# Performance work log

Hardware: AMD Instinct MI355X
Metric: run time of the kernel (lower is better)

## Reference

```python
import jax, jax.numpy as jnp
import numpy as np

N_ATOMS, N_UND, N_DIR, N_ANG, N_STRUCT = 8192, 65536, 131072, 262144, 128
FEA, NRAD, NANGB, NCONV = 64, 9, 9, 4

FLOAT_NAMES = ["bond_bases_ag", "bond_bases_bg", "angle_bases", "atom_emb", "Wb", "Wa",
               "Wbw_ag", "Wbw_bg",
               "ac_cw1", "ac_cb1", "ac_cw2", "ac_cb2", "ac_gw1", "ac_gb1", "ac_gw2", "ac_gb2", "ac_out",
               "bc_cw1", "bc_cb1", "bc_cw2", "bc_cb2", "bc_gw1", "bc_gb1", "bc_gw2", "bc_gb2", "bc_out",
               "an_cw", "an_cb", "an_gw", "an_gb",
               "ro_w1", "ro_b1", "ro_w2", "ro_b2", "ro_w3", "ro_b3"]
INT_NAMES = ["atomic_numbers", "atom_graph", "directed2undirected",
             "bond_graph_atoms", "bond_graph_bonds", "atom_owners"]


def _silu(x):
    return x * jax.nn.sigmoid(x)


def _gmlp(x, cw1, cb1, cw2, cb2, gw1, gb1, gw2, gb2):
    # GatedMLP (norm=None): silu(MLP_core(x)) * sigmoid(MLP_gate(x)), each MLP = Lin-silu-Lin
    core = _silu(_silu(x @ cw1 + cb1) @ cw2 + cb2)
    gate = jax.nn.sigmoid(_silu(x @ gw1 + gb1) @ gw2 + gb2)
    return core * gate


def _forward(F, I):
    seg = jax.ops.segment_sum
    atom = F["atom_emb"][I["atomic_numbers"]]            # [N, 64]
    bond = F["bond_bases_ag"] @ F["Wb"]                  # [U, 64]
    angle = F["angle_bases"] @ F["Wa"]                   # [A, 64]
    bw_ag = F["bond_bases_ag"] @ F["Wbw_ag"]             # [U, 64]
    bw_bg = F["bond_bases_bg"] @ F["Wbw_bg"]             # [U, 64]
    ag0, ag1 = I["atom_graph"][:, 0], I["atom_graph"][:, 1]
    d2u = I["directed2undirected"]
    bgi, bgj = I["bond_graph_bonds"][:, 0], I["bond_graph_bonds"][:, 1]
    bga = I["bond_graph_atoms"]

    def atom_conv(i, atom, bond):
        msg = jnp.concatenate([atom[ag0], bond[d2u], atom[ag1]], axis=1)   # [E, 192]
        msg = _gmlp(msg, F["ac_cw1"][i], F["ac_cb1"][i], F["ac_cw2"][i], F["ac_cb2"][i],
                    F["ac_gw1"][i], F["ac_gb1"][i], F["ac_gw2"][i], F["ac_gb2"][i])
        msg = msg * bw_ag[d2u]
        # scatter-add to center atoms, linear mlp_out (no bias), resnet
        return atom + seg(msg, ag0, num_segments=N_ATOMS) @ F["ac_out"][i]

    for i in range(NCONV - 1):
        atom = atom_conv(i, atom, bond)
        # BondConv over bond graph (angles)
        tot = jnp.concatenate([bond[bgi], bond[bgj], angle, atom[bga]], axis=1)  # [A, 256]
        upd = _gmlp(tot, F["bc_cw1"][i], F["bc_cb1"][i], F["bc_cw2"][i], F["bc_cb2"][i],
                    F["bc_gw1"][i], F["bc_gb1"][i], F["bc_gw2"][i], F["bc_gb2"][i])
        upd = upd * bw_bg[bgi]
        bond = bond + seg(upd, bgi, num_segments=N_UND) @ F["bc_out"][i]
        # AngleUpdate (hidden_dim=0 -> single linear in each gated branch), resnet
        tot2 = jnp.concatenate([bond[bgi], bond[bgj], angle, atom[bga]], axis=1)
        angle = angle + _silu(tot2 @ F["an_cw"][i] + F["an_cb"][i]) * \
            jax.nn.sigmoid(tot2 @ F["an_gw"][i] + F["an_gb"][i])
    atom = atom_conv(NCONV - 1, atom, bond)

    # mlp_first readout: per-atom energy MLP then average pooling per structure
    e = _silu(atom @ F["ro_w1"] + F["ro_b1"])
    e = _silu(e @ F["ro_w2"] + F["ro_b2"])
    e = (e @ F["ro_w3"] + F["ro_b3"])[:, 0]              # [N]
    owners = I["atom_owners"]
    esum = seg(e, owners, num_segments=N_STRUCT)
    cnt = seg(jnp.ones_like(e), owners, num_segments=N_STRUCT)
    return esum / jnp.maximum(cnt, 1.0)                  # [N_STRUCT] energy/atom


def setup_inputs() -> dict:
    key = jax.random.key(0)
    ks = iter(jax.random.split(key, 64))

    def nrm(shape, fan_in):
        return jax.random.normal(next(ks), shape, dtype=jnp.float32) / np.float32(np.sqrt(fan_in))

    z = lambda *s: jnp.zeros(s, dtype=jnp.float32)
    inp = {}
    inp["atomic_numbers"] = jax.random.randint(next(ks), (N_ATOMS,), 0, 94, dtype=jnp.int32)
    inp["bond_bases_ag"] = jax.random.uniform(next(ks), (N_UND, NRAD), dtype=jnp.float32)
    inp["bond_bases_bg"] = jax.random.uniform(next(ks), (N_UND, NRAD), dtype=jnp.float32)
    inp["angle_bases"] = jax.random.uniform(next(ks), (N_ANG, NANGB), dtype=jnp.float32)
    inp["atom_graph"] = jax.random.randint(next(ks), (N_DIR, 2), 0, N_ATOMS, dtype=jnp.int32)
    inp["directed2undirected"] = jax.random.randint(next(ks), (N_DIR,), 0, N_UND, dtype=jnp.int32)
    inp["bond_graph_atoms"] = jax.random.randint(next(ks), (N_ANG,), 0, N_ATOMS, dtype=jnp.int32)
    inp["bond_graph_bonds"] = jax.random.randint(next(ks), (N_ANG, 2), 0, N_UND, dtype=jnp.int32)
    inp["atom_owners"] = jnp.sort(jax.random.randint(next(ks), (N_ATOMS,), 0, N_STRUCT, dtype=jnp.int32))
    inp["atom_emb"] = nrm((95, FEA), 1.0)
    inp["Wb"] = nrm((NRAD, FEA), NRAD)
    inp["Wa"] = nrm((NANGB, FEA), NANGB)
    inp["Wbw_ag"] = nrm((NRAD, FEA), NRAD)
    inp["Wbw_bg"] = nrm((NRAD, FEA), NRAD)
    d_a, d_b = 3 * FEA, 4 * FEA
    nb = NCONV - 1
    inp["ac_cw1"] = nrm((NCONV, d_a, FEA), d_a); inp["ac_cb1"] = z(NCONV, FEA)
    inp["ac_cw2"] = nrm((NCONV, FEA, FEA), FEA); inp["ac_cb2"] = z(NCONV, FEA)
    inp["ac_gw1"] = nrm((NCONV, d_a, FEA), d_a); inp["ac_gb1"] = z(NCONV, FEA)
    inp["ac_gw2"] = nrm((NCONV, FEA, FEA), FEA); inp["ac_gb2"] = z(NCONV, FEA)
    inp["ac_out"] = nrm((NCONV, FEA, FEA), FEA)
    inp["bc_cw1"] = nrm((nb, d_b, FEA), d_b); inp["bc_cb1"] = z(nb, FEA)
    inp["bc_cw2"] = nrm((nb, FEA, FEA), FEA); inp["bc_cb2"] = z(nb, FEA)
    inp["bc_gw1"] = nrm((nb, d_b, FEA), d_b); inp["bc_gb1"] = z(nb, FEA)
    inp["bc_gw2"] = nrm((nb, FEA, FEA), FEA); inp["bc_gb2"] = z(nb, FEA)
    inp["bc_out"] = nrm((nb, FEA, FEA), FEA)
    inp["an_cw"] = nrm((nb, d_b, FEA), d_b); inp["an_cb"] = z(nb, FEA)
    inp["an_gw"] = nrm((nb, d_b, FEA), d_b); inp["an_gb"] = z(nb, FEA)
    inp["ro_w1"] = nrm((FEA, FEA), FEA); inp["ro_b1"] = z(FEA)
    inp["ro_w2"] = nrm((FEA, FEA), FEA); inp["ro_b2"] = z(FEA)
    inp["ro_w3"] = nrm((FEA, 1), FEA); inp["ro_b3"] = z(1)
    return inp


def reference(atomic_numbers, bond_bases_ag, bond_bases_bg, angle_bases, atom_graph,
              directed2undirected, bond_graph_atoms, bond_graph_bonds, atom_owners,
              atom_emb, Wb, Wa, Wbw_ag, Wbw_bg,
              ac_cw1, ac_cb1, ac_cw2, ac_cb2, ac_gw1, ac_gb1, ac_gw2, ac_gb2, ac_out,
              bc_cw1, bc_cb1, bc_cw2, bc_cb2, bc_gw1, bc_gb1, bc_gw2, bc_gb2, bc_out,
              an_cw, an_cb, an_gw, an_gb,
              ro_w1, ro_b1, ro_w2, ro_b2, ro_w3, ro_b3):
    loc = locals()
    F = {k: loc[k] for k in FLOAT_NAMES}
    I = {k: loc[k] for k in INT_NAMES}
    return _forward(F, I)
```

## Files before the change

### kernel.cpp

```cpp
#include <hip/hip_runtime.h>
#include <hip/hip_bf16.h>

typedef float f32x4 __attribute__((ext_vector_type(4)));
typedef short s16x8 __attribute__((ext_vector_type(8)));
typedef unsigned int u32x4 __attribute__((ext_vector_type(4)));

#define DEV static __device__ __forceinline__

DEV unsigned short f2bf(float x){
    unsigned u = __builtin_bit_cast(unsigned, x);
    u += 0x7FFFu + ((u >> 16) & 1u);
    return (unsigned short)(u >> 16);
}
DEV float bf2f(unsigned short h){
    unsigned u = ((unsigned)h) << 16;
    return __builtin_bit_cast(float, u);
}
DEV float sigm_(float x){ return __builtin_amdgcn_rcpf(1.0f + __expf(-x)); }
DEV float silu_(float x){ return x * sigm_(x); }

__global__ __launch_bounds__(256) void k_transconv(const float* __restrict__ src,
                                                   unsigned short* __restrict__ dst,
                                                   int K, int total){
    int gid = blockIdx.x * 256 + threadIdx.x;
    if (gid >= total) return;
    int kn  = K * 64;
    int b   = gid / kn;
    int rem = gid - b * kn;
    int k   = rem >> 6, n = rem & 63;
    dst[b * kn + n * K + k] = f2bf(src[gid]);
}

__global__ __launch_bounds__(256) void k_embed(const float* __restrict__ emb,
                                               const int* __restrict__ z,
                                               unsigned short* __restrict__ out){
    int gid = blockIdx.x * 256 + threadIdx.x;
    int n = gid >> 6, f = gid & 63;
    out[gid] = f2bf(emb[z[n] * 64 + f]);
}

__global__ __launch_bounds__(256) void k_smallmm(const float* __restrict__ bases,
                                                 const float* __restrict__ W,
                                                 unsigned short* __restrict__ out){
    int gid = blockIdx.x * 256 + threadIdx.x;
    int r = gid >> 6, f = gid & 63;
    const float* b = bases + r * 9;
    float acc = 0.f;
    #pragma unroll
    for (int k = 0; k < 9; ++k) acc += b[k] * W[k * 64 + f];
    out[gid] = f2bf(acc);
}

__global__ void k_count(const int* __restrict__ dst, int stride, int n, int* __restrict__ cnt){
    int i = blockIdx.x * 256 + threadIdx.x;
    if (i < n) atomicAdd(&cnt[dst[(size_t)i * stride]], 1);
}

__global__ __launch_bounds__(256) void k_bsum(const int* __restrict__ cnt,
                                              int* __restrict__ bsum){
    int i = blockIdx.x * 256 + threadIdx.x;
    int v = cnt[i];
    #pragma unroll
    for (int off = 32; off > 0; off >>= 1) v += __shfl_down(v, off);
    __shared__ int ws[4];
    if ((threadIdx.x & 63) == 0) ws[threadIdx.x >> 6] = v;
    __syncthreads();
    if (threadIdx.x == 0) bsum[blockIdx.x] = ws[0] + ws[1] + ws[2] + ws[3];
}

__global__ __launch_bounds__(256) void k_bscan(const int* __restrict__ bsum,
                                               int* __restrict__ bbase, int nb,
                                               int* __restrict__ total_out){
    __shared__ int sh[256];
    int t = threadIdx.x;
    int v = (t < nb) ? bsum[t] : 0;
    sh[t] = v;
    __syncthreads();
    for (int d = 1; d < 256; d <<= 1){
        int u = (t >= d) ? sh[t - d] : 0;
        __syncthreads();
        sh[t] += u;
        __syncthreads();
    }
    if (t < nb) bbase[t] = sh[t] - v;
    if (t == nb - 1) *total_out = sh[t];
}

__global__ __launch_bounds__(256) void k_offs(const int* __restrict__ cnt,
                                              const int* __restrict__ bbase,
                                              int* __restrict__ offs){
    __shared__ int sh[256];
    int t = threadIdx.x;
    int i = blockIdx.x * 256 + t;
    int v = cnt[i];
    sh[t] = v;
    __syncthreads();
    for (int d = 1; d < 256; d <<= 1){
        int u = (t >= d) ? sh[t - d] : 0;
        __syncthreads();
        sh[t] += u;
        __syncthreads();
    }
    offs[i] = bbase[blockIdx.x] + sh[t] - v;
}

__global__ void k_fill(const int* __restrict__ dst, int stride, int n,
                       const int* __restrict__ offs, int* __restrict__ cur,
                       int* __restrict__ idx){
    int i = blockIdx.x * 256 + threadIdx.x;
    if (i < n){
        int d = dst[(size_t)i * stride];
        int p = offs[d] + atomicAdd(&cur[d], 1);
        idx[p] = i;
    }
}

__global__ __launch_bounds__(256) void k_reduce(const unsigned short* __restrict__ upd,
                                                const int* __restrict__ offs,
                                                const int* __restrict__ idx,
                                                unsigned short* __restrict__ act, int nRows){
    int gid = blockIdx.x * 256 + threadIdx.x;
    int row = gid >> 3;
    if (row >= nRows) return;
    int c8 = (gid & 7) * 8;
    int o = offs[row], e = offs[row + 1];
    float acc[8] = {};
    for (int j = o; j < e; ++j){
        s16x8 v = *(const s16x8*)&upd[(size_t)idx[j] * 64 + c8];
        #pragma unroll
        for (int q = 0; q < 8; ++q) acc[q] += bf2f((unsigned short)v[q]);
    }
    s16x8 a = *(s16x8*)&act[(size_t)row * 64 + c8];
    #pragma unroll
    for (int q = 0; q < 8; ++q) a[q] = (short)f2bf(bf2f((unsigned short)a[q]) + acc[q]);
    *(s16x8*)&act[(size_t)row * 64 + c8] = a;
}

#define MFMA16(a,b,c) __builtin_amdgcn_mfma_f32_16x16x32_bf16(a,b,c,0,0,0)

__global__ __launch_bounds__(256, 4) void k_atom_conv(
    const unsigned short* __restrict__ atomBf, const unsigned short* __restrict__ bondBf,
    const unsigned short* __restrict__ bwagBf,
    const int* __restrict__ agraph, const int* __restrict__ d2u,
    const unsigned short* __restrict__ w1cT, const unsigned short* __restrict__ w1gT,
    const unsigned short* __restrict__ w2cT, const unsigned short* __restrict__ w2gT,
    const unsigned short* __restrict__ woT,
    const float* __restrict__ cb1, const float* __restrict__ cb2,
    const float* __restrict__ gb1, const float* __restrict__ gb2,
    unsigned short* __restrict__ upd)
{
    __shared__ unsigned short lds[14208];
    __shared__ int ldsIdx[64];
    unsigned short* ldsA  = lds;
    unsigned short* ldsHC = lds;
    unsigned short* ldsHG = lds + 4736;
    unsigned short* ldsV  = lds + 9472;
    const int tid = threadIdx.x;
    const int r0  = blockIdx.x * 64;

    {
        const int srow = tid >> 2, q = tid & 3;
        int e = r0 + srow;
        if (q < 3){
            const unsigned short* src;
            if (q == 0)      src = atomBf + (size_t)agraph[2 * e] * 64;
            else if (q == 1){ int u = d2u[e]; ldsIdx[srow] = u; src = bondBf + (size_t)u * 64; }
            else             src = atomBf + (size_t)agraph[2 * e + 1] * 64;
            #pragma unroll
            for (int j = 0; j < 8; ++j)
                *(u32x4*)&ldsA[srow * 200 + q * 64 + j * 8] = *(const u32x4*)(src + j * 8);
        }
    }
    __syncthreads();

    const int lane = tid & 63;
    const int r16  = lane & 15;
    const int grp  = lane >> 4;
    const int col  = (tid >> 6) * 16 + r16;

    unsigned short bwv[16];
    #pragma unroll
    for (int mt = 0; mt < 4; ++mt)
        #pragma unroll
        for (int j = 0; j < 4; ++j)
            bwv[mt * 4 + j] = bwagBf[(size_t)ldsIdx[mt * 16 + grp * 4 + j] * 64 + col];

    f32x4 aC[4] = {}, aG[4] = {};
    #pragma unroll
    for (int kt = 0; kt < 6; ++kt){
        s16x8 bc = *(const s16x8*)&w1cT[col * 192 + kt * 32 + grp * 8];
        s16x8 bg = *(const s16x8*)&w1gT[col * 192 + kt * 32 + grp * 8];
        #pragma unroll
        for (int mt = 0; mt < 4; ++mt){
            s16x8 a = *(const s16x8*)&ldsA[(mt * 16 + r16) * 200 + kt * 32 + grp * 8];
            aC[mt] = MFMA16(a, bc, aC[mt]);
            aG[mt] = MFMA16(a, bg, aG[mt]);
        }
    }
    __syncthreads();

    const float bC1 = cb1[col], bG1 = gb1[col];
    #pragma unroll
    for (int mt = 0; mt < 4; ++mt){
        #pragma unroll
        for (int j = 0; j < 4; ++j){
            int row = mt * 16 + grp * 4 + j;
            ldsHC[row * 74 + col] = f2bf(silu_(aC[mt][j] + bC1));
            ldsHG[row * 74 + col] = f2bf(silu_(aG[mt][j] + bG1));
        }
    }
    __syncthreads();

    f32x4 oC[4] = {}, oG[4] = {};
    #pragma unroll
    for (int kt = 0; kt < 2; ++kt){
        s16x8 bc = *(const s16x8*)&w2cT[col * 64 + kt * 32 + grp * 8];
        s16x8 bg = *(const s16x8*)&w2gT[col * 64 + kt * 32 + grp * 8];
        #pragma unroll
        for (int mt = 0; mt < 4; ++mt){
            s16x8 hc = *(const s16x8*)&ldsHC[(mt * 16 + r16) * 74 + kt * 32 + grp * 8];
            s16x8 hg = *(const s16x8*)&ldsHG[(mt * 16 + r16) * 74 + kt * 32 + grp * 8];
            oC[mt] = MFMA16(hc, bc, oC[mt]);
            oG[mt] = MFMA16(hg, bg, oG[mt]);
        }
    }
    const float bC2 = cb2[col], bG2 = gb2[col];
    #pragma unroll
    for (int mt = 0; mt < 4; ++mt){
        #pragma unroll
        for (int j = 0; j < 4; ++j){
            int row = mt * 16 + grp * 4 + j;
            float v = silu_(oC[mt][j] + bC2) * sigm_(oG[mt][j] + bG2);
            v *= bf2f(bwv[mt * 4 + j]);
            ldsV[row * 74 + col] = f2bf(v);
        }
    }
    __syncthreads();

    f32x4 oD[4] = {};
    #pragma unroll
    for (int kt = 0; kt < 2; ++kt){
        s16x8 bo = *(const s16x8*)&woT[col * 64 + kt * 32 + grp * 8];
        #pragma unroll
        for (int mt = 0; mt < 4; ++mt){
            s16x8 a = *(const s16x8*)&ldsV[(mt * 16 + r16) * 74 + kt * 32 + grp * 8];
            oD[mt] = MFMA16(a, bo, oD[mt]);
        }
    }
    #pragma unroll
    for (int mt = 0; mt < 4; ++mt){
        #pragma unroll
        for (int j = 0; j < 4; ++j){
            int row = mt * 16 + grp * 4 + j;
            upd[(size_t)(r0 + row) * 64 + col] = f2bf(oD[mt][j]);
        }
    }
}

__global__ __launch_bounds__(256, 4) void k_bond_conv(
    const unsigned short* __restrict__ atomBf, const unsigned short* __restrict__ bondBf,
    const unsigned short* __restrict__ angleBf, const unsigned short* __restrict__ bwbgBf,
    const int* __restrict__ bga, const int* __restrict__ bgb,
    const unsigned short* __restrict__ w1cT, const unsigned short* __restrict__ w1gT,
    const unsigned short* __restrict__ w2cT, const unsigned short* __restrict__ w2gT,
    const unsigned short* __restrict__ woT,
    const float* __restrict__ cb1, const float* __restrict__ cb2,
    const float* __restrict__ gb1, const float* __restrict__ gb2,
    unsigned short* __restrict__ upd)
{
    __shared__ unsigned short lds[16896];
    __shared__ int ldsIdx[64];
    unsigned short* ldsA  = lds;
    unsigned short* ldsHC = lds;
    unsigned short* ldsHG = lds + 4736;
    unsigned short* ldsV  = lds + 9472;
    const int tid = threadIdx.x;
    const int r0  = blockIdx.x * 64;

    {
        const int srow = tid >> 2, q = tid & 3;
        int a = r0 + srow;
        const unsigned short* src;
        if (q == 0){ int2 bb = *(const int2*)&bgb[2 * a]; ldsIdx[srow] = bb.x;
                     src = bondBf + (size_t)bb.x * 64; }
        else if (q == 1){ src = bondBf  + (size_t)bgb[2 * a + 1] * 64; }
        else if (q == 2){ src = angleBf + (size_t)a * 64; }
        else            { src = atomBf  + (size_t)bga[a] * 64; }
        #pragma unroll
        for (int j = 0; j < 8; ++j)
            *(u32x4*)&ldsA[srow * 264 + q * 64 + j * 8] = *(const u32x4*)(src + j * 8);
    }
    __syncthreads();

    const int lane = tid & 63;
    const int r16  = lane & 15;
    const int grp  = lane >> 4;
    const int col  = (tid >> 6) * 16 + r16;

    unsigned short bwv[16];
    #pragma unroll
    for (int mt = 0; mt < 4; ++mt)
        #pragma unroll
        for (int j = 0; j < 4; ++j)
            bwv[mt * 4 + j] = bwbgBf[(size_t)ldsIdx[mt * 16 + grp * 4 + j] * 64 + col];

    f32x4 aC[4] = {}, aG[4] = {};
    #pragma unroll
    for (int kt = 0; kt < 8; ++kt){
        s16x8 bc = *(const s16x8*)&w1cT[col * 256 + kt * 32 + grp * 8];
        s16x8 bg = *(const s16x8*)&w1gT[col * 256 + kt * 32 + grp * 8];
        #pragma unroll
        for (int mt = 0; mt < 4; ++mt){
            s16x8 a = *(const s16x8*)&ldsA[(mt * 16 + r16) * 264 + kt * 32 + grp * 8];
            aC[mt] = MFMA16(a, bc, aC[mt]);
            aG[mt] = MFMA16(a, bg, aG[mt]);
        }
    }
    __syncthreads();

    const float bC1 = cb1[col], bG1 = gb1[col];
    #pragma unroll
    for (int mt = 0; mt < 4; ++mt){
        #pragma unroll
        for (int j = 0; j < 4; ++j){
            int row = mt * 16 + grp * 4 + j;
            ldsHC[row * 74 + col] = f2bf(silu_(aC[mt][j] + bC1));
            ldsHG[row * 74 + col] = f2bf(silu_(aG[mt][j] + bG1));
        }
    }
    __syncthreads();

    f32x4 oC[4] = {}, oG[4] = {};
    #pragma unroll
    for (int kt = 0; kt < 2; ++kt){
        s16x8 bc = *(const s16x8*)&w2cT[col * 64 + kt * 32 + grp * 8];
        s16x8 bg = *(const s16x8*)&w2gT[col * 64 + kt * 32 + grp * 8];
        #pragma unroll
        for (int mt = 0; mt < 4; ++mt){
            s16x8 hc = *(const s16x8*)&ldsHC[(mt * 16 + r16) * 74 + kt * 32 + grp * 8];
            s16x8 hg = *(const s16x8*)&ldsHG[(mt * 16 + r16) * 74 + kt * 32 + grp * 8];
            oC[mt] = MFMA16(hc, bc, oC[mt]);
            oG[mt] = MFMA16(hg, bg, oG[mt]);
        }
    }
    const float bC2 = cb2[col], bG2 = gb2[col];
    #pragma unroll
    for (int mt = 0; mt < 4; ++mt){
        #pragma unroll
        for (int j = 0; j < 4; ++j){
            int row = mt * 16 + grp * 4 + j;
            float v = silu_(oC[mt][j] + bC2) * sigm_(oG[mt][j] + bG2);
            v *= bf2f(bwv[mt * 4 + j]);
            ldsV[row * 74 + col] = f2bf(v);
        }
    }
    __syncthreads();

    f32x4 oD[4] = {};
    #pragma unroll
    for (int kt = 0; kt < 2; ++kt){
        s16x8 bo = *(const s16x8*)&woT[col * 64 + kt * 32 + grp * 8];
        #pragma unroll
        for (int mt = 0; mt < 4; ++mt){
            s16x8 a = *(const s16x8*)&ldsV[(mt * 16 + r16) * 74 + kt * 32 + grp * 8];
            oD[mt] = MFMA16(a, bo, oD[mt]);
        }
    }
    #pragma unroll
    for (int mt = 0; mt < 4; ++mt){
        #pragma unroll
        for (int j = 0; j < 4; ++j){
            int row = mt * 16 + grp * 4 + j;
            upd[(size_t)(r0 + row) * 64 + col] = f2bf(oD[mt][j]);
        }
    }
}

__global__ __launch_bounds__(256, 4) void k_angle(
    const unsigned short* __restrict__ atomBf, const unsigned short* __restrict__ bondBf,
    unsigned short* __restrict__ angleBf,
    const int* __restrict__ bga, const int* __restrict__ bgb,
    const unsigned short* __restrict__ wcT, const unsigned short* __restrict__ wgT,
    const float* __restrict__ cb, const float* __restrict__ gb)
{
    __shared__ unsigned short ldsA[64 * 264];
    const int tid = threadIdx.x;
    const int r0  = blockIdx.x * 64;

    {
        const int srow = tid >> 2, q = tid & 3;
        int a = r0 + srow;
        const unsigned short* src;
        if (q == 0)      src = bondBf  + (size_t)bgb[2 * a] * 64;
        else if (q == 1) src = bondBf  + (size_t)bgb[2 * a + 1] * 64;
        else if (q == 2) src = angleBf + (size_t)a * 64;
        else             src = atomBf  + (size_t)bga[a] * 64;
        #pragma unroll
        for (int j = 0; j < 8; ++j)
            *(u32x4*)&ldsA[srow * 264 + q * 64 + j * 8] = *(const u32x4*)(src + j * 8);
    }
    __syncthreads();

    const int lane = tid & 63;
    const int r16  = lane & 15;
    const int grp  = lane >> 4;
    const int col  = (tid >> 6) * 16 + r16;

    f32x4 aC[4] = {}, aG[4] = {};
    #pragma unroll
    for (int kt = 0; kt < 8; ++kt){
        s16x8 bc = *(const s16x8*)&wcT[col * 256 + kt * 32 + grp * 8];
        s16x8 bg = *(const s16x8*)&wgT[col * 256 + kt * 32 + grp * 8];
        #pragma unroll
        for (int mt = 0; mt < 4; ++mt){
            s16x8 a = *(const s16x8*)&ldsA[(mt * 16 + r16) * 264 + kt * 32 + grp * 8];
            aC[mt] = MFMA16(a, bc, aC[mt]);
            aG[mt] = MFMA16(a, bg, aG[mt]);
        }
    }
    const float bC = cb[col], bG = gb[col];
    #pragma unroll
    for (int mt = 0; mt < 4; ++mt){
        #pragma unroll
        for (int j = 0; j < 4; ++j){
            int row = mt * 16 + grp * 4 + j;
            int a = r0 + row;
            float oldv = bf2f(ldsA[row * 264 + 128 + col]);
            float v = silu_(aC[mt][j] + bC) * sigm_(aG[mt][j] + bG);
            angleBf[(size_t)a * 64 + col] = f2bf(oldv + v);
        }
    }
}

__global__ __launch_bounds__(256) void k_readout(
    const unsigned short* __restrict__ atomBf, const int* __restrict__ owners,
    const float* __restrict__ w1, const float* __restrict__ b1,
    const float* __restrict__ w2, const float* __restrict__ b2,
    const float* __restrict__ w3, const float* __restrict__ b3,
    float* __restrict__ esum, float* __restrict__ cnt)
{
    int gid  = blockIdx.x * 256 + threadIdx.x;
    int n    = gid >> 6;
    int lane = threadIdx.x & 63;
    float a = bf2f(atomBf[n * 64 + lane]);
    float acc = b1[lane];
    #pragma unroll
    for (int k = 0; k < 64; ++k) acc += __shfl(a, k) * w1[k * 64 + lane];
    float h = silu_(acc);
    acc = b2[lane];
    #pragma unroll
    for (int k = 0; k < 64; ++k) acc += __shfl(h, k) * w2[k * 64 + lane];
    h = silu_(acc);
    float p = h * w3[lane];
    #pragma unroll
    for (int off = 32; off > 0; off >>= 1) p += __shfl_xor(p, off);
    if (lane == 0){
        atomicAdd(&esum[owners[n]], p + b3[0]);
        atomicAdd(&cnt[owners[n]], 1.0f);
    }
}

__global__ void k_final(const float* __restrict__ esum, const float* __restrict__ cnt,
                        float* __restrict__ out){
    int i = threadIdx.x;
    if (i < 128) out[i] = esum[i] / fmaxf(cnt[i], 1.0f);
}

extern "C" void kernel_launch(void* const* d_in, const int* in_sizes, int n_in,
                              void* d_out, int out_size, void* d_ws, size_t ws_size,
                              hipStream_t stream)
{
    (void)in_sizes; (void)n_in; (void)out_size; (void)ws_size;
    const int N_ATOMS = 8192, N_UND = 65536, N_DIR = 131072, N_ANG = 262144;

    const int*   atomic_numbers = (const int*)  d_in[0];
    const float* bb_ag  = (const float*)d_in[1];
    const float* bb_bg  = (const float*)d_in[2];
    const float* ang_b  = (const float*)d_in[3];
    const int*   agraph = (const int*)  d_in[4];
    const int*   d2u    = (const int*)  d_in[5];
    const int*   bga    = (const int*)  d_in[6];
    const int*   bgb    = (const int*)  d_in[7];
    const int*   owners = (const int*)  d_in[8];
    const float* emb    = (const float*)d_in[9];
    const float* Wb     = (const float*)d_in[10];
    const float* Wa     = (const float*)d_in[11];
    const float* Wbwag  = (const float*)d_in[12];
    const float* Wbwbg  = (const float*)d_in[13];
    const float* ac_cw1 = (const float*)d_in[14];
    const float* ac_cb1 = (const float*)d_in[15];
    const float* ac_cw2 = (const float*)d_in[16];
    const float* ac_cb2 = (const float*)d_in[17];
    const float* ac_gw1 = (const float*)d_in[18];
    const float* ac_gb1 = (const float*)d_in[19];
    const float* ac_gw2 = (const float*)d_in[20];
    const float* ac_gb2 = (const float*)d_in[21];
    const float* ac_out = (const float*)d_in[22];
    const float* bc_cw1 = (const float*)d_in[23];
    const float* bc_cb1 = (const float*)d_in[24];
    const float* bc_cw2 = (const float*)d_in[25];
    const float* bc_cb2 = (const float*)d_in[26];
    const float* bc_gw1 = (const float*)d_in[27];
    const float* bc_gb1 = (const float*)d_in[28];
    const float* bc_gw2 = (const float*)d_in[29];
    const float* bc_gb2 = (const float*)d_in[30];
    const float* bc_out = (const float*)d_in[31];
    const float* an_cw  = (const float*)d_in[32];
    const float* an_cb  = (const float*)d_in[33];
    const float* an_gw  = (const float*)d_in[34];
    const float* an_gb  = (const float*)d_in[35];
    const float* ro_w1  = (const float*)d_in[36];
    const float* ro_b1  = (const float*)d_in[37];
    const float* ro_w2  = (const float*)d_in[38];
    const float* ro_b2  = (const float*)d_in[39];
    const float* ro_w3  = (const float*)d_in[40];
    const float* ro_b3  = (const float*)d_in[41];

    char* ws = (char*)d_ws;
    size_t off = 0;
    auto alloc = [&](size_t bytes) -> void* {
        void* p = ws + off;
        off = (off + bytes + 255) & ~(size_t)255;
        return p;
    };
    unsigned short* atomBf  = (unsigned short*)alloc((size_t)N_ATOMS * 64 * 2);
    unsigned short* bondBf  = (unsigned short*)alloc((size_t)N_UND   * 64 * 2);
    unsigned short* angleBf = (unsigned short*)alloc((size_t)N_ANG   * 64 * 2);
    unsigned short* bwagBf  = (unsigned short*)alloc((size_t)N_UND   * 64 * 2);
    unsigned short* bwbgBf  = (unsigned short*)alloc((size_t)N_UND   * 64 * 2);
    unsigned short* updBuf  = (unsigned short*)alloc((size_t)N_ANG   * 64 * 2);
    float* esum   = (float*)alloc(128 * 4);
    float* cnt    = (float*)alloc(128 * 4);
    int* offsA = (int*)alloc((N_ATOMS + 1) * 4);
    int* curA  = (int*)alloc(N_ATOMS * 4);
    int* idxA  = (int*)alloc((size_t)N_DIR * 4);
    int* offsB = (int*)alloc((N_UND + 1) * 4);
    int* curB  = (int*)alloc(N_UND * 4);
    int* idxB  = (int*)alloc((size_t)N_ANG * 4);
    int* bsum  = (int*)alloc(256 * 4);
    int* bbase = (int*)alloc(256 * 4);
    unsigned short* acw1cT = (unsigned short*)alloc((size_t)4 * 64 * 192 * 2);
    unsigned short* acw1gT = (unsigned short*)alloc((size_t)4 * 64 * 192 * 2);
    unsigned short* acw2cT = (unsigned short*)alloc((size_t)4 * 64 * 64 * 2);
    unsigned short* acw2gT = (unsigned short*)alloc((size_t)4 * 64 * 64 * 2);
    unsigned short* acoT   = (unsigned short*)alloc((size_t)4 * 64 * 64 * 2);
    unsigned short* bcw1cT = (unsigned short*)alloc((size_t)3 * 64 * 256 * 2);
    unsigned short* bcw1gT = (unsigned short*)alloc((size_t)3 * 64 * 256 * 2);
    unsigned short* bcw2cT = (unsigned short*)alloc((size_t)3 * 64 * 64 * 2);
    unsigned short* bcw2gT = (unsigned short*)alloc((size_t)3 * 64 * 64 * 2);
    unsigned short* bcoT   = (unsigned short*)alloc((size_t)3 * 64 * 64 * 2);
    unsigned short* anwcT  = (unsigned short*)alloc((size_t)3 * 64 * 256 * 2);
    unsigned short* anwgT  = (unsigned short*)alloc((size_t)3 * 64 * 256 * 2);

    auto tc = [&](const float* src, unsigned short* dst, int B, int K){
        int total = B * K * 64;
        k_transconv<<<(total + 255) / 256, 256, 0, stream>>>(src, dst, K, total);
    };
    tc(ac_cw1, acw1cT, 4, 192);  tc(ac_gw1, acw1gT, 4, 192);
    tc(ac_cw2, acw2cT, 4, 64);   tc(ac_gw2, acw2gT, 4, 64);
    tc(ac_out, acoT,   4, 64);
    tc(bc_cw1, bcw1cT, 3, 256);  tc(bc_gw1, bcw1gT, 3, 256);
    tc(bc_cw2, bcw2cT, 3, 64);   tc(bc_gw2, bcw2gT, 3, 64);
    tc(bc_out, bcoT,   3, 64);
    tc(an_cw,  anwcT,  3, 256);  tc(an_gw,  anwgT,  3, 256);

    k_embed<<<N_ATOMS * 64 / 256, 256, 0, stream>>>(emb, atomic_numbers, atomBf);
    k_smallmm<<<N_UND * 64 / 256, 256, 0, stream>>>(bb_ag, Wb,    bondBf);
    k_smallmm<<<N_ANG * 64 / 256, 256, 0, stream>>>(ang_b, Wa,    angleBf);
    k_smallmm<<<N_UND * 64 / 256, 256, 0, stream>>>(bb_ag, Wbwag, bwagBf);
    k_smallmm<<<N_UND * 64 / 256, 256, 0, stream>>>(bb_bg, Wbwbg, bwbgBf);

    hipMemsetAsync(curA, 0, N_ATOMS * 4, stream);
    k_count<<<(N_DIR + 255) / 256, 256, 0, stream>>>(agraph, 2, N_DIR, curA);
    k_bsum <<<N_ATOMS / 256, 256, 0, stream>>>(curA, bsum);
    k_bscan<<<1, 256, 0, stream>>>(bsum, bbase, N_ATOMS / 256, offsA + N_ATOMS);
    k_offs <<<N_ATOMS / 256, 256, 0, stream>>>(curA, bbase, offsA);
    hipMemsetAsync(curA, 0, N_ATOMS * 4, stream);
    k_fill<<<(N_DIR + 255) / 256, 256, 0, stream>>>(agraph, 2, N_DIR, offsA, curA, idxA);

    hipMemsetAsync(curB, 0, N_UND * 4, stream);
    k_count<<<(N_ANG + 255) / 256, 256, 0, stream>>>(bgb, 2, N_ANG, curB);
    k_bsum <<<N_UND / 256, 256, 0, stream>>>(curB, bsum);
    k_bscan<<<1, 256, 0, stream>>>(bsum, bbase, N_UND / 256, offsB + N_UND);
    k_offs <<<N_UND / 256, 256, 0, stream>>>(curB, bbase, offsB);
    hipMemsetAsync(curB, 0, N_UND * 4, stream);
    k_fill<<<(N_ANG + 255) / 256, 256, 0, stream>>>(bgb, 2, N_ANG, offsB, curB, idxB);

    for (int i = 0; i < 4; ++i){
        k_atom_conv<<<N_DIR / 64, 256, 0, stream>>>(
            atomBf, bondBf, bwagBf, agraph, d2u,
            acw1cT + (size_t)i * 64 * 192, acw1gT + (size_t)i * 64 * 192,
            acw2cT + (size_t)i * 64 * 64,  acw2gT + (size_t)i * 64 * 64,
            acoT   + (size_t)i * 64 * 64,
            ac_cb1 + i * 64, ac_cb2 + i * 64, ac_gb1 + i * 64, ac_gb2 + i * 64, updBuf);
        k_reduce<<<N_ATOMS * 8 / 256, 256, 0, stream>>>(updBuf, offsA, idxA, atomBf, N_ATOMS);
        if (i == 3) break;
        k_bond_conv<<<N_ANG / 64, 256, 0, stream>>>(
            atomBf, bondBf, angleBf, bwbgBf, bga, bgb,
            bcw1cT + (size_t)i * 64 * 256, bcw1gT + (size_t)i * 64 * 256,
            bcw2cT + (size_t)i * 64 * 64,  bcw2gT + (size_t)i * 64 * 64,
            bcoT   + (size_t)i * 64 * 64,
            bc_cb1 + i * 64, bc_cb2 + i * 64, bc_gb1 + i * 64, bc_gb2 + i * 64, updBuf);
        k_reduce<<<N_UND * 8 / 256, 256, 0, stream>>>(updBuf, offsB, idxB, bondBf, N_UND);
        k_angle<<<N_ANG / 64, 256, 0, stream>>>(
            atomBf, bondBf, angleBf, bga, bgb,
            anwcT + (size_t)i * 64 * 256, anwgT + (size_t)i * 64 * 256,
            an_cb + i * 64, an_gb + i * 64);
    }

    hipMemsetAsync(esum, 0, 128 * 4, stream);
    hipMemsetAsync(cnt,  0, 128 * 4, stream);
    k_readout<<<N_ATOMS * 64 / 256, 256, 0, stream>>>(
        atomBf, owners, ro_w1, ro_b1, ro_w2, ro_b2, ro_w3, ro_b3, esum, cnt);
    k_final<<<1, 128, 0, stream>>>(esum, cnt, (float*)d_out);
}
```

Before: 913.2 us.

## Process edges in sorted order and prefetch next tile gathers across persistent tiles

The edge kernels now walk edges in destination-sorted order (via idxA/idxB), so updates land contiguously and the reduce kernel reads rows directly without an index indirection. Each block handles several 64-row tiles, prefetching the next tile's gathered rows into registers while computing the current one. The atom-conv bond weights are staged through LDS. The change also adds extra index indirection in the gathers, fewer blocks, and higher register pressure, and the angle kernel now does scattered writes.

```diff
diff --git a/kernel.cpp b/kernel.cpp
--- a/kernel.cpp
+++ b/kernel.cpp
@@ -117,7 +117,6 @@
 
 __global__ __launch_bounds__(256) void k_reduce(const unsigned short* __restrict__ upd,
                                                 const int* __restrict__ offs,
-                                                const int* __restrict__ idx,
                                                 unsigned short* __restrict__ act, int nRows){
     int gid = blockIdx.x * 256 + threadIdx.x;
     int row = gid >> 3;
@@ -126,7 +125,7 @@
     int o = offs[row], e = offs[row + 1];
     float acc[8] = {};
     for (int j = o; j < e; ++j){
-        s16x8 v = *(const s16x8*)&upd[(size_t)idx[j] * 64 + c8];
+        s16x8 v = *(const s16x8*)&upd[(size_t)j * 64 + c8];
         #pragma unroll
         for (int q = 0; q < 8; ++q) acc[q] += bf2f((unsigned short)v[q]);
     }
@@ -137,11 +136,13 @@
 }
 
 #define MFMA16(a,b,c) __builtin_amdgcn_mfma_f32_16x16x32_bf16(a,b,c,0,0,0)
+#define TB 4
 
 __global__ __launch_bounds__(256, 4) void k_atom_conv(
     const unsigned short* __restrict__ atomBf, const unsigned short* __restrict__ bondBf,
     const unsigned short* __restrict__ bwagBf,
     const int* __restrict__ agraph, const int* __restrict__ d2u,
+    const int* __restrict__ idxA,
     const unsigned short* __restrict__ w1cT, const unsigned short* __restrict__ w1gT,
     const unsigned short* __restrict__ w2cT, const unsigned short* __restrict__ w2gT,
     const unsigned short* __restrict__ woT,
@@ -150,110 +151,121 @@
     unsigned short* __restrict__ upd)
 {
     __shared__ unsigned short lds[14208];
-    __shared__ int ldsIdx[64];
+    __shared__ unsigned short ldsBw[64 * 68];
     unsigned short* ldsA  = lds;
     unsigned short* ldsHC = lds;
     unsigned short* ldsHG = lds + 4736;
     unsigned short* ldsV  = lds + 9472;
-    const int tid = threadIdx.x;
-    const int r0  = blockIdx.x * 64;
-
-    {
-        const int srow = tid >> 2, q = tid & 3;
-        int e = r0 + srow;
-        if (q < 3){
+    const int tid   = threadIdx.x;
+    const int lane8 = tid & 7;
+    const int sb    = tid >> 3;
+    const int lane  = tid & 63;
+    const int r16   = lane & 15;
+    const int grp   = lane >> 4;
+    const int col   = (tid >> 6) * 16 + r16;
+
+    u32x4 pre[8];
+    auto resolve = [&](int rbase){
+        #pragma unroll
+        for (int p = 0; p < 8; ++p){
+            int sid = p * 32 + sb;
+            int q = sid >> 6, row = sid & 63;
+            int e = idxA[rbase + row];
             const unsigned short* src;
             if (q == 0)      src = atomBf + (size_t)agraph[2 * e] * 64;
-            else if (q == 1){ int u = d2u[e]; ldsIdx[srow] = u; src = bondBf + (size_t)u * 64; }
-            else             src = atomBf + (size_t)agraph[2 * e + 1] * 64;
-            #pragma unroll
-            for (int j = 0; j < 8; ++j)
-                *(u32x4*)&ldsA[srow * 200 + q * 64 + j * 8] = *(const u32x4*)(src + j * 8);
-        }
-    }
-    __syncthreads();
-
-    const int lane = tid & 63;
-    const int r16  = lane & 15;
-    const int grp  = lane >> 4;
-    const int col  = (tid >> 6) * 16 + r16;
-
-    unsigned short bwv[16];
-    #pragma unroll
-    for (int mt = 0; mt < 4; ++mt)
-        #pragma unroll
-        for (int j = 0; j < 4; ++j)
-            bwv[mt * 4 + j] = bwagBf[(size_t)ldsIdx[mt * 16 + grp * 4 + j] * 64 + col];
-
-    f32x4 aC[4] = {}, aG[4] = {};
-    #pragma unroll
-    for (int kt = 0; kt < 6; ++kt){
-        s16x8 bc = *(const s16x8*)&w1cT[col * 192 + kt * 32 + grp * 8];
-        s16x8 bg = *(const s16x8*)&w1gT[col * 192 + kt * 32 + grp * 8];
+            else if (q == 1) src = bondBf + (size_t)d2u[e] * 64;
+            else if (q == 2) src = atomBf + (size_t)agraph[2 * e + 1] * 64;
+            else             src = bwagBf + (size_t)d2u[e] * 64;
+            pre[p] = *(const u32x4*)(src + lane8 * 8);
+        }
+    };
+
+    const int base = blockIdx.x * (TB * 64);
+    resolve(base);
+    const float bC1 = cb1[col], bG1 = gb1[col];
+    const float bC2 = cb2[col], bG2 = gb2[col];
+
+    for (int t = 0; t < TB; ++t){
+        const int r0 = base + t * 64;
+        #pragma unroll
+        for (int p = 0; p < 8; ++p){
+            int sid = p * 32 + sb;
+            int q = sid >> 6, row = sid & 63;
+            if (q < 3) *(u32x4*)&ldsA[row * 200 + q * 64 + lane8 * 8] = pre[p];
+            else       *(u32x4*)&ldsBw[row * 68 + lane8 * 8] = pre[p];
+        }
+        __syncthreads();
+        if (t < TB - 1) resolve(base + (t + 1) * 64);
+
+        f32x4 aC[4] = {}, aG[4] = {};
+        #pragma unroll
+        for (int kt = 0; kt < 6; ++kt){
+            s16x8 bc = *(const s16x8*)&w1cT[col * 192 + kt * 32 + grp * 8];
+            s16x8 bg = *(const s16x8*)&w1gT[col * 192 + kt * 32 + grp * 8];
+            #pragma unroll
+            for (int mt = 0; mt < 4; ++mt){
+                s16x8 a = *(const s16x8*)&ldsA[(mt * 16 + r16) * 200 + kt * 32 + grp * 8];
+                aC[mt] = MFMA16(a, bc, aC[mt]);
+                aG[mt] = MFMA16(a, bg, aG[mt]);
+            }
+        }
+        __syncthreads();
+
         #pragma unroll
         for (int mt = 0; mt < 4; ++mt){
-            s16x8 a = *(const s16x8*)&ldsA[(mt * 16 + r16) * 200 + kt * 32 + grp * 8];
-            aC[mt] = MFMA16(a, bc, aC[mt]);
-            aG[mt] = MFMA16(a, bg, aG[mt]);
-        }
-    }
-    __syncthreads();
-
-    const float bC1 = cb1[col], bG1 = gb1[col];
-    #pragma unroll
-    for (int mt = 0; mt < 4; ++mt){
-        #pragma unroll
-        for (int j = 0; j < 4; ++j){
-            int row = mt * 16 + grp * 4 + j;
-            ldsHC[row * 74 + col] = f2bf(silu_(aC[mt][j] + bC1));
-            ldsHG[row * 74 + col] = f2bf(silu_(aG[mt][j] + bG1));
-        }
-    }
-    __syncthreads();
-
-    f32x4 oC[4] = {}, oG[4] = {};
-    #pragma unroll
-    for (int kt = 0; kt < 2; ++kt){
-        s16x8 bc = *(const s16x8*)&w2cT[col * 64 + kt * 32 + grp * 8];
-        s16x8 bg = *(const s16x8*)&w2gT[col * 64 + kt * 32 + grp * 8];
+            #pragma unroll
+            for (int j = 0; j < 4; ++j){
+                int row = mt * 16 + grp * 4 + j;
+                ldsHC[row * 74 + col] = f2bf(silu_(aC[mt][j] + bC1));
+                ldsHG[row * 74 + col] = f2bf(silu_(aG[mt][j] + bG1));
+            }
+        }
+        __syncthreads();
+
+        f32x4 oC[4] = {}, oG[4] = {};
+        #pragma unroll
+        for (int kt = 0; kt < 2; ++kt){
+            s16x8 bc = *(const s16x8*)&w2cT[col * 64 + kt * 32 + grp * 8];
+            s16x8 bg = *(const s16x8*)&w2gT[col * 64 + kt * 32 + grp * 8];
+            #pragma unroll
+            for (int mt = 0; mt < 4; ++mt){
+                s16x8 hc = *(const s16x8*)&ldsHC[(mt * 16 + r16) * 74 + kt * 32 + grp * 8];
+                s16x8 hg = *(const s16x8*)&ldsHG[(mt * 16 + r16) * 74 + kt * 32 + grp * 8];
+                oC[mt] = MFMA16(hc, bc, oC[mt]);
+                oG[mt] = MFMA16(hg, bg, oG[mt]);
+            }
+        }
         #pragma unroll
         for (int mt = 0; mt < 4; ++mt){
-            s16x8 hc = *(const s16x8*)&ldsHC[(mt * 16 + r16) * 74 + kt * 32 + grp * 8];
-            s16x8 hg = *(const s16x8*)&ldsHG[(mt * 16 + r16) * 74 + kt * 32 + grp * 8];
-            oC[mt] = MFMA16(hc, bc, oC[mt]);
-            oG[mt] = MFMA16(hg, bg, oG[mt]);
-        }
-    }
-    const float bC2 = cb2[col], bG2 = gb2[col];
-    #pragma unroll
-    for (int mt = 0; mt < 4; ++mt){
-        #pragma unroll
-        for (int j = 0; j < 4; ++j){
-            int row = mt * 16 + grp * 4 + j;
-            float v = silu_(oC[mt][j] + bC2) * sigm_(oG[mt][j] + bG2);
-            v *= bf2f(bwv[mt * 4 + j]);
-            ldsV[row * 74 + col] = f2bf(v);
-        }
-    }
-    __syncthreads();
-
-    f32x4 oD[4] = {};
-    #pragma unroll
-    for (int kt = 0; kt < 2; ++kt){
-        s16x8 bo = *(const s16x8*)&woT[col * 64 + kt * 32 + grp * 8];
+            #pragma unroll
+            for (int j = 0; j < 4; ++j){
+                int row = mt * 16 + grp * 4 + j;
+                float v = silu_(oC[mt][j] + bC2) * sigm_(oG[mt][j] + bG2);
+                v *= bf2f(ldsBw[row * 68 + col]);
+                ldsV[row * 74 + col] = f2bf(v);
+            }
+        }
+        __syncthreads();
+
+        f32x4 oD[4] = {};
+        #pragma unroll
+        for (int kt = 0; kt < 2; ++kt){
+            s16x8 bo = *(const s16x8*)&woT[col * 64 + kt * 32 + grp * 8];
+            #pragma unroll
+            for (int mt = 0; mt < 4; ++mt){
+                s16x8 a = *(const s16x8*)&ldsV[(mt * 16 + r16) * 74 + kt * 32 + grp * 8];
+                oD[mt] = MFMA16(a, bo, oD[mt]);
+            }
+        }
         #pragma unroll
         for (int mt = 0; mt < 4; ++mt){
-            s16x8 a = *(const s16x8*)&ldsV[(mt * 16 + r16) * 74 + kt * 32 + grp * 8];
-            oD[mt] = MFMA16(a, bo, oD[mt]);
-        }
-    }
-    #pragma unroll
-    for (int mt = 0; mt < 4; ++mt){
-        #pragma unroll
-        for (int j = 0; j < 4; ++j){
-            int row = mt * 16 + grp * 4 + j;
-            upd[(size_t)(r0 + row) * 64 + col] = f2bf(oD[mt][j]);
-        }
+            #pragma unroll
+            for (int j = 0; j < 4; ++j){
+                int row = mt * 16 + grp * 4 + j;
+                upd[(size_t)(r0 + row) * 64 + col] = f2bf(oD[mt][j]);
+            }
+        }
+        __syncthreads();
     }
 }
 
@@ -261,6 +273,7 @@
     const unsigned short* __restrict__ atomBf, const unsigned short* __restrict__ bondBf,
     const unsigned short* __restrict__ angleBf, const unsigned short* __restrict__ bwbgBf,
     const int* __restrict__ bga, const int* __restrict__ bgb,
+    const int* __restrict__ idxB,
     const unsigned short* __restrict__ w1cT, const unsigned short* __restrict__ w1gT,
     const unsigned short* __restrict__ w2cT, const unsigned short* __restrict__ w2gT,
     const unsigned short* __restrict__ woT,
@@ -274,105 +287,125 @@
     unsigned short* ldsHC = lds;
     unsigned short* ldsHG = lds + 4736;
     unsigned short* ldsV  = lds + 9472;
-    const int tid = threadIdx.x;
-    const int r0  = blockIdx.x * 64;
-
-    {
-        const int srow = tid >> 2, q = tid & 3;
-        int a = r0 + srow;
-        const unsigned short* src;
-        if (q == 0){ int2 bb = *(const int2*)&bgb[2 * a]; ldsIdx[srow] = bb.x;
-                     src = bondBf + (size_t)bb.x * 64; }
-        else if (q == 1){ src = bondBf  + (size_t)bgb[2 * a + 1] * 64; }
-        else if (q == 2){ src = angleBf + (size_t)a * 64; }
-        else            { src = atomBf  + (size_t)bga[a] * 64; }
-        #pragma unroll
-        for (int j = 0; j < 8; ++j)
-            *(u32x4*)&ldsA[srow * 264 + q * 64 + j * 8] = *(const u32x4*)(src + j * 8);
-    }
-    __syncthreads();
-
-    const int lane = tid & 63;
-    const int r16  = lane & 15;
-    const int grp  = lane >> 4;
-    const int col  = (tid >> 6) * 16 + r16;
-
-    unsigned short bwv[16];
-    #pragma unroll
-    for (int mt = 0; mt < 4; ++mt)
-        #pragma unroll
-        for (int j = 0; j < 4; ++j)
-            bwv[mt * 4 + j] = bwbgBf[(size_t)ldsIdx[mt * 16 + grp * 4 + j] * 64 + col];
-
-    f32x4 aC[4] = {}, aG[4] = {};
-    #pragma unroll
-    for (int kt = 0; kt < 8; ++kt){
-        s16x8 bc = *(const s16x8*)&w1cT[col * 256 + kt * 32 + grp * 8];
-        s16x8 bg = *(const s16x8*)&w1gT[col * 256 + kt * 32 + grp * 8];
+    const int tid   = threadIdx.x;
+    const int lane8 = tid & 7;
+    const int sb    = tid >> 3;
+    const int lane  = tid & 63;
+    const int r16   = lane & 15;
+    const int grp   = lane >> 4;
+    const int col   = (tid >> 6) * 16 + r16;
+
+    u32x4 pre[8];
+    int nIdx = 0;
+    auto resolve = [&](int rbase){
+        #pragma unroll
+        for (int p = 0; p < 8; ++p){
+            int sid = p * 32 + sb;
+            int q = sid >> 6, row = sid & 63;
+            int a = idxB[rbase + row];
+            const unsigned short* src;
+            if (q == 0)      src = bondBf  + (size_t)bgb[2 * a] * 64;
+            else if (q == 1) src = bondBf  + (size_t)bgb[2 * a + 1] * 64;
+            else if (q == 2) src = angleBf + (size_t)a * 64;
+            else             src = atomBf  + (size_t)bga[a] * 64;
+            pre[p] = *(const u32x4*)(src + lane8 * 8);
+        }
+        if (tid < 64) nIdx = bgb[2 * idxB[rbase + tid]];
+    };
+
+    const int base = blockIdx.x * (TB * 64);
+    resolve(base);
+    const float bC1 = cb1[col], bG1 = gb1[col];
+    const float bC2 = cb2[col], bG2 = gb2[col];
+
+    for (int t = 0; t < TB; ++t){
+        const int r0 = base + t * 64;
+        #pragma unroll
+        for (int p = 0; p < 8; ++p){
+            int sid = p * 32 + sb;
+            int q = sid >> 6, row = sid & 63;
+            *(u32x4*)&ldsA[row * 264 + q * 64 + lane8 * 8] = pre[p];
+        }
+        if (tid < 64) ldsIdx[tid] = nIdx;
+        __syncthreads();
+
+        unsigned short bwv[16];
+        #pragma unroll
+        for (int mt = 0; mt < 4; ++mt)
+            #pragma unroll
+            for (int j = 0; j < 4; ++j)
+                bwv[mt * 4 + j] = bwbgBf[(size_t)ldsIdx[mt * 16 + grp * 4 + j] * 64 + col];
+        if (t < TB - 1) resolve(base + (t + 1) * 64);
+
+        f32x4 aC[4] = {}, aG[4] = {};
+        #pragma unroll
+        for (int kt = 0; kt < 8; ++kt){
+            s16x8 bc = *(const s16x8*)&w1cT[col * 256 + kt * 32 + grp * 8];
+            s16x8 bg = *(const s16x8*)&w1gT[col * 256 + kt * 32 + grp * 8];
+            #pragma unroll
+            for (int mt = 0; mt < 4; ++mt){
+                s16x8 a = *(const s16x8*)&ldsA[(mt * 16 + r16) * 264 + kt * 32 + grp * 8];
+                aC[mt] = MFMA16(a, bc, aC[mt]);
+                aG[mt] = MFMA16(a, bg, aG[mt]);
+            }
+        }
+        __syncthreads();
+
         #pragma unroll
         for (int mt = 0; mt < 4; ++mt){
-            s16x8 a = *(const s16x8*)&ldsA[(mt * 16 + r16) * 264 + kt * 32 + grp * 8];
-            aC[mt] = MFMA16(a, bc, aC[mt]);
-            aG[mt] = MFMA16(a, bg, aG[mt]);
-        }
-    }
-    __syncthreads();
-
-    const float bC1 = cb1[col], bG1 = gb1[col];
-    #pragma unroll
-    for (int mt = 0; mt < 4; ++mt){
-        #pragma unroll
-        for (int j = 0; j < 4; ++j){
-            int row = mt * 16 + grp * 4 + j;
-            ldsHC[row * 74 + col] = f2bf(silu_(aC[mt][j] + bC1));
-            ldsHG[row * 74 + col] = f2bf(silu_(aG[mt][j] + bG1));
-        }
-    }
-    __syncthreads();
-
-    f32x4 oC[4] = {}, oG[4] = {};
-    #pragma unroll
-    for (int kt = 0; kt < 2; ++kt){
-        s16x8 bc = *(const s16x8*)&w2cT[col * 64 + kt * 32 + grp * 8];
-        s16x8 bg = *(const s16x8*)&w2gT[col * 64 + kt * 32 + grp * 8];
+            #pragma unroll
+            for (int j = 0; j < 4; ++j){
+                int row = mt * 16 + grp * 4 + j;
+                ldsHC[row * 74 + col] = f2bf(silu_(aC[mt][j] + bC1));
+                ldsHG[row * 74 + col] = f2bf(silu_(aG[mt][j] + bG1));
+            }
+        }
+        __syncthreads();
+
+        f32x4 oC[4] = {}, oG[4] = {};
+        #pragma unroll
+        for (int kt = 0; kt < 2; ++kt){
+            s16x8 bc = *(const s16x8*)&w2cT[col * 64 + kt * 32 + grp * 8];
+            s16x8 bg = *(const s16x8*)&w2gT[col * 64 + kt * 32 + grp * 8];
+            #pragma unroll
+            for (int mt = 0; mt < 4; ++mt){
+                s16x8 hc = *(const s16x8*)&ldsHC[(mt * 16 + r16) * 74 + kt * 32 + grp * 8];
+                s16x8 hg = *(const s16x8*)&ldsHG[(mt * 16 + r16) * 74 + kt * 32 + grp * 8];
+                oC[mt] = MFMA16(hc, bc, oC[mt]);
+                oG[mt] = MFMA16(hg, bg, oG[mt]);
+            }
+        }
         #pragma unroll
         for (int mt = 0; mt < 4; ++mt){
-            s16x8 hc = *(const s16x8*)&ldsHC[(mt * 16 + r16) * 74 + kt * 32 + grp * 8];
-            s16x8 hg = *(const s16x8*)&ldsHG[(mt * 16 + r16) * 74 + kt * 32 + grp * 8];
-            oC[mt] = MFMA16(hc, bc, oC[mt]);
-            oG[mt] = MFMA16(hg, bg, oG[mt]);
-        }
-    }
-    const float bC2 = cb2[col], bG2 = gb2[col];
-    #pragma unroll
-    for (int mt = 0; mt < 4; ++mt){
-        #pragma unroll
-        for (int j = 0; j < 4; ++j){
-            int row = mt * 16 + grp * 4 + j;
-            float v = silu_(oC[mt][j] + bC2) * sigm_(oG[mt][j] + bG2);
-            v *= bf2f(bwv[mt * 4 + j]);
-            ldsV[row * 74 + col] = f2bf(v);
-        }
-    }
-    __syncthreads();
-
-    f32x4 oD[4] = {};
-    #pragma unroll
-    for (int kt = 0; kt < 2; ++kt){
-        s16x8 bo = *(const s16x8*)&woT[col * 64 + kt * 32 + grp * 8];
+            #pragma unroll
+            for (int j = 0; j < 4; ++j){
+                int row = mt * 16 + grp * 4 + j;
+                float v = silu_(oC[mt][j] + bC2) * sigm_(oG[mt][j] + bG2);
+                v *= bf2f(bwv[mt * 4 + j]);
+                ldsV[row * 74 + col] = f2bf(v);
+            }
+        }
+        __syncthreads();
+
+        f32x4 oD[4] = {};
+        #pragma unroll
+        for (int kt = 0; kt < 2; ++kt){
+            s16x8 bo = *(const s16x8*)&woT[col * 64 + kt * 32 + grp * 8];
+            #pragma unroll
+            for (int mt = 0; mt < 4; ++mt){
+                s16x8 a = *(const s16x8*)&ldsV[(mt * 16 + r16) * 74 + kt * 32 + grp * 8];
+                oD[mt] = MFMA16(a, bo, oD[mt]);
+            }
+        }
         #pragma unroll
         for (int mt = 0; mt < 4; ++mt){
-            s16x8 a = *(const s16x8*)&ldsV[(mt * 16 + r16) * 74 + kt * 32 + grp * 8];
-            oD[mt] = MFMA16(a, bo, oD[mt]);
-        }
-    }
-    #pragma unroll
-    for (int mt = 0; mt < 4; ++mt){
-        #pragma unroll
-        for (int j = 0; j < 4; ++j){
-            int row = mt * 16 + grp * 4 + j;
-            upd[(size_t)(r0 + row) * 64 + col] = f2bf(oD[mt][j]);
-        }
+            #pragma unroll
+            for (int j = 0; j < 4; ++j){
+                int row = mt * 16 + grp * 4 + j;
+                upd[(size_t)(r0 + row) * 64 + col] = f2bf(oD[mt][j]);
+            }
+        }
+        __syncthreads();
     }
 }
 
@@ -380,55 +413,76 @@
     const unsigned short* __restrict__ atomBf, const unsigned short* __restrict__ bondBf,
     unsigned short* __restrict__ angleBf,
     const int* __restrict__ bga, const int* __restrict__ bgb,
+    const int* __restrict__ idxB,
     const unsigned short* __restrict__ wcT, const unsigned short* __restrict__ wgT,
     const float* __restrict__ cb, const float* __restrict__ gb)
 {
     __shared__ unsigned short ldsA[64 * 264];
-    const int tid = threadIdx.x;
-    const int r0  = blockIdx.x * 64;
-
-    {
-        const int srow = tid >> 2, q = tid & 3;
-        int a = r0 + srow;
-        const unsigned short* src;
-        if (q == 0)      src = bondBf  + (size_t)bgb[2 * a] * 64;
-        else if (q == 1) src = bondBf  + (size_t)bgb[2 * a + 1] * 64;
-        else if (q == 2) src = angleBf + (size_t)a * 64;
-        else             src = atomBf  + (size_t)bga[a] * 64;
-        #pragma unroll
-        for (int j = 0; j < 8; ++j)
-            *(u32x4*)&ldsA[srow * 264 + q * 64 + j * 8] = *(const u32x4*)(src + j * 8);
-    }
-    __syncthreads();
-
-    const int lane = tid & 63;
-    const int r16  = lane & 15;
-    const int grp  = lane >> 4;
-    const int col  = (tid >> 6) * 16 + r16;
-
-    f32x4 aC[4] = {}, aG[4] = {};
-    #pragma unroll
-    for (int kt = 0; kt < 8; ++kt){
-        s16x8 bc = *(const s16x8*)&wcT[col * 256 + kt * 32 + grp * 8];
-        s16x8 bg = *(const s16x8*)&wgT[col * 256 + kt * 32 + grp * 8];
+    __shared__ int ldsIdx[64];
+    const int tid   = threadIdx.x;
+    const int lane8 = tid & 7;
+    const int sb    = tid >> 3;
+    const int lane  = tid & 63;
+    const int r16   = lane & 15;
+    const int grp   = lane >> 4;
+    const int col   = (tid >> 6) * 16 + r16;
+
+    u32x4 pre[8];
+    int nIdx = 0;
+    auto resolve = [&](int rbase){
+        #pragma unroll
+        for (int p = 0; p < 8; ++p){
+            int sid = p * 32 + sb;
+            int q = sid >> 6, row = sid & 63;
+            int a = idxB[rbase + row];
+            const unsigned short* src;
+            if (q == 0)      src = bondBf  + (size_t)bgb[2 * a] * 64;
+            else if (q == 1) src = bondBf  + (size_t)bgb[2 * a + 1] * 64;
+            else if (q == 2) src = angleBf + (size_t)a * 64;
+            else             src = atomBf  + (size_t)bga[a] * 64;
+            pre[p] = *(const u32x4*)(src + lane8 * 8);
+        }
+        if (tid < 64) nIdx = idxB[rbase + tid];
+    };
+
+    const int base = blockIdx.x * (TB * 64);
+    resolve(base);
+    const float bC = cb[col], bG = gb[col];
+
+    for (int t = 0; t < TB; ++t){
+        #pragma unroll
+        for (int p = 0; p < 8; ++p){
+            int sid = p * 32 + sb;
+            int q = sid >> 6, row = sid & 63;
+            *(u32x4*)&ldsA[row * 264 + q * 64 + lane8 * 8] = pre[p];
+        }
+        if (tid < 64) ldsIdx[tid] = nIdx;
+        __syncthreads();
+        if (t < TB - 1) resolve(base + (t + 1) * 64);
+
+        f32x4 aC[4] = {}, aG[4] = {};
+        #pragma unroll
+        for (int kt = 0; kt < 8; ++kt){
+            s16x8 bc = *(const s16x8*)&wcT[col * 256 + kt * 32 + grp * 8];
+            s16x8 bg = *(const s16x8*)&wgT[col * 256 + kt * 32 + grp * 8];
+            #pragma unroll
+            for (int mt = 0; mt < 4; ++mt){
+                s16x8 a = *(const s16x8*)&ldsA[(mt * 16 + r16) * 264 + kt * 32 + grp * 8];
+                aC[mt] = MFMA16(a, bc, aC[mt]);
+                aG[mt] = MFMA16(a, bg, aG[mt]);
+            }
+        }
         #pragma unroll
         for (int mt = 0; mt < 4; ++mt){
-            s16x8 a = *(const s16x8*)&ldsA[(mt * 16 + r16) * 264 + kt * 32 + grp * 8];
-            aC[mt] = MFMA16(a, bc, aC[mt]);
-            aG[mt] = MFMA16(a, bg, aG[mt]);
-        }
-    }
-    const float bC = cb[col], bG = gb[col];
-    #pragma unroll
-    for (int mt = 0; mt < 4; ++mt){
-        #pragma unroll
-        for (int j = 0; j < 4; ++j){
-            int row = mt * 16 + grp * 4 + j;
-            int a = r0 + row;
-            float oldv = bf2f(ldsA[row * 264 + 128 + col]);
-            float v = silu_(aC[mt][j] + bC) * sigm_(aG[mt][j] + bG);
-            angleBf[(size_t)a * 64 + col] = f2bf(oldv + v);
-        }
+            #pragma unroll
+            for (int j = 0; j < 4; ++j){
+                int row = mt * 16 + grp * 4 + j;
+                float oldv = bf2f(ldsA[row * 264 + 128 + col]);
+                float v = silu_(aC[mt][j] + bC) * sigm_(aG[mt][j] + bG);
+                angleBf[(size_t)ldsIdx[row] * 64 + col] = f2bf(oldv + v);
+            }
+        }
+        __syncthreads();
     }
 }
 
@@ -587,23 +641,23 @@
     k_fill<<<(N_ANG + 255) / 256, 256, 0, stream>>>(bgb, 2, N_ANG, offsB, curB, idxB);
 
     for (int i = 0; i < 4; ++i){
-        k_atom_conv<<<N_DIR / 64, 256, 0, stream>>>(
-            atomBf, bondBf, bwagBf, agraph, d2u,
+        k_atom_conv<<<N_DIR / (64 * TB), 256, 0, stream>>>(
+            atomBf, bondBf, bwagBf, agraph, d2u, idxA,
             acw1cT + (size_t)i * 64 * 192, acw1gT + (size_t)i * 64 * 192,
             acw2cT + (size_t)i * 64 * 64,  acw2gT + (size_t)i * 64 * 64,
             acoT   + (size_t)i * 64 * 64,
             ac_cb1 + i * 64, ac_cb2 + i * 64, ac_gb1 + i * 64, ac_gb2 + i * 64, updBuf);
-        k_reduce<<<N_ATOMS * 8 / 256, 256, 0, stream>>>(updBuf, offsA, idxA, atomBf, N_ATOMS);
+        k_reduce<<<N_ATOMS * 8 / 256, 256, 0, stream>>>(updBuf, offsA, atomBf, N_ATOMS);
         if (i == 3) break;
-        k_bond_conv<<<N_ANG / 64, 256, 0, stream>>>(
-            atomBf, bondBf, angleBf, bwbgBf, bga, bgb,
+        k_bond_conv<<<N_ANG / (64 * TB), 256, 0, stream>>>(
+            atomBf, bondBf, angleBf, bwbgBf, bga, bgb, idxB,
             bcw1cT + (size_t)i * 64 * 256, bcw1gT + (size_t)i * 64 * 256,
             bcw2cT + (size_t)i * 64 * 64,  bcw2gT + (size_t)i * 64 * 64,
             bcoT   + (size_t)i * 64 * 64,
             bc_cb1 + i * 64, bc_cb2 + i * 64, bc_gb1 + i * 64, bc_gb2 + i * 64, updBuf);
-        k_reduce<<<N_UND * 8 / 256, 256, 0, stream>>>(updBuf, offsB, idxB, bondBf, N_UND);
-        k_angle<<<N_ANG / 64, 256, 0, stream>>>(
-            atomBf, bondBf, angleBf, bga, bgb,
+        k_reduce<<<N_UND * 8 / 256, 256, 0, stream>>>(updBuf, offsB, bondBf, N_UND);
+        k_angle<<<N_ANG / (64 * TB), 256, 0, stream>>>(
+            atomBf, bondBf, angleBf, bga, bgb, idxB,
             anwcT + (size_t)i * 64 * 256, anwgT + (size_t)i * 64 * 256,
             an_cb + i * 64, an_gb + i * 64);
     }
```

Result: slower. 1.423 ms (+55.8%).
